# Kernel tuning notes

Hardware: AMD Instinct MI355X
Metric: run time of the kernel (lower is better)

Reference implementation:

```python
import jax, jax.numpy as jnp
import numpy as np

N = 20000       # nodes
E = 320000      # edges (before self-loops)
F_IN = 1024     # num_features
H = 4           # head_num
C = 64          # hidden_size
NC = 4          # n_classes
NEG_SLOPE = 0.2 # PyG GATConv default


def setup_inputs() -> dict:
    key = jax.random.key(0)
    ks = jax.random.split(key, 16)
    def w(k, shape, fan_in):
        return jax.random.normal(k, shape, dtype=jnp.float32) / np.sqrt(fan_in)
    x = jax.random.normal(ks[0], (N, F_IN), dtype=jnp.float32)
    edge_index = jax.random.randint(ks[1], (2, E), 0, N, dtype=jnp.int64)
    return {
        "x": x,
        "edge_index": edge_index,
        # layer 1: F_IN -> H*C, concat
        "w1": w(ks[2], (F_IN, H * C), F_IN),
        "as1": w(ks[3], (H, C), C),
        "ad1": w(ks[4], (H, C), C),
        "b1": jnp.zeros((H * C,), jnp.float32),
        # layer 2: H*C -> H*C, concat
        "w2": w(ks[5], (H * C, H * C), H * C),
        "as2": w(ks[6], (H, C), C),
        "ad2": w(ks[7], (H, C), C),
        "b2": jnp.zeros((H * C,), jnp.float32),
        # out layer: H*C -> C, 1 head, concat=False
        "w3": w(ks[8], (H * C, 1 * C), H * C),
        "as3": w(ks[9], (1, C), C),
        "ad3": w(ks[10], (1, C), C),
        "b3": jnp.zeros((C,), jnp.float32),
        # classifier
        "wc": w(ks[11], (C, NC), C),
        "bc": jnp.zeros((NC,), jnp.float32),
    }


def gat_layer(x, src, dst, W, a_src, a_dst, bias, concat):
    """PyG GATConv (eval mode, self-loops already added to src/dst)."""
    n = x.shape[0]
    Hh, Cc = a_src.shape
    h = (x @ W).reshape(n, Hh, Cc)                       # [N,H,C]
    al_s = jnp.sum(h * a_src[None], axis=-1)             # [N,H]
    al_d = jnp.sum(h * a_dst[None], axis=-1)             # [N,H]
    e = al_s[src] + al_d[dst]                            # [E,H]
    e = jax.nn.leaky_relu(e, NEG_SLOPE)
    # segment softmax over incoming edges of each destination node
    emax = jax.ops.segment_max(e, dst, num_segments=n)   # [N,H]
    ex = jnp.exp(e - emax[dst])
    denom = jax.ops.segment_sum(ex, dst, num_segments=n) # [N,H]
    alpha = ex / (denom[dst] + 1e-16)                    # [E,H]
    msg = h[src] * alpha[..., None]                      # [E,H,C]
    out = jax.ops.segment_sum(msg, dst, num_segments=n)  # [N,H,C]
    if concat:
        out = out.reshape(n, Hh * Cc)
    else:
        out = out.mean(axis=1)
    return out + bias


def reference(x, edge_index, w1, as1, ad1, b1, w2, as2, ad2, b2,
              w3, as3, ad3, b3, wc, bc):
    n = x.shape[0]
    loop = jnp.arange(n, dtype=edge_index.dtype)
    src = jnp.concatenate([edge_index[0], loop])
    dst = jnp.concatenate([edge_index[1], loop])
    out = jax.nn.relu(gat_layer(x, src, dst, w1, as1, ad1, b1, True))
    out = jax.nn.relu(gat_layer(out, src, dst, w2, as2, ad2, b2, True))
    out = gat_layer(out, src, dst, w3, as3, ad3, b3, False)
    return out @ wc + bc                                  # [N, n_classes]
```

## Files before the change

kernel.cpp:

```cpp
#include <hip/hip_runtime.h>

#define N_NODES 20000
#define N_EDGES 320000
#define ET (N_EDGES + N_NODES)
#define F_IN 1024
#define HC 256
#define NC 4

typedef unsigned short ushort_t;
typedef __attribute__((ext_vector_type(8))) short short8;
typedef __attribute__((ext_vector_type(4))) float f32x4;

__device__ inline ushort_t f2bf(float f) {
    unsigned u = __float_as_uint(f);
    unsigned r = (u + 0x7fffu + ((u >> 16) & 1u)) >> 16;
    return (ushort_t)r;
}
__device__ inline float bf2f(ushort_t u) {
    return __uint_as_float(((unsigned)u) << 16);
}

__device__ inline unsigned cvt_pk_bf16(float lo, float hi) {
    unsigned r;
    asm("v_cvt_pk_bf16_f32 %0, %1, %2" : "=v"(r) : "v"(lo), "v"(hi));
    return r;
}

#define GLOAD16(gp, lp) __builtin_amdgcn_global_load_lds( \
    (const __attribute__((address_space(1))) void*)(gp),  \
    (__attribute__((address_space(3))) void*)(lp), 16, 0, 0)

__global__ void count_kernel(const int* __restrict__ ei, int* __restrict__ counts) {
    int e = blockIdx.x * blockDim.x + threadIdx.x;
    if (e >= ET) return;
    int dst = (e < N_EDGES) ? ei[N_EDGES + e] : (e - N_EDGES);
    atomicAdd(&counts[dst], 1);
}

__global__ void scan_kernel(const int* __restrict__ counts, int* __restrict__ row_ptr,
                            int* __restrict__ cursor) {
    __shared__ int sums[1024];
    int t = threadIdx.x;
    const int per = (N_NODES + 1023) / 1024;
    int b = t * per;
    int e = min(b + per, N_NODES);
    int s = 0;
    for (int i = b; i < e; ++i) s += counts[i];
    sums[t] = s;
    __syncthreads();
    for (int off = 1; off < 1024; off <<= 1) {
        int v = (t >= off) ? sums[t - off] : 0;
        __syncthreads();
        sums[t] += v;
        __syncthreads();
    }
    int run = (t == 0) ? 0 : sums[t - 1];
    for (int i = b; i < e; ++i) {
        row_ptr[i] = run;
        cursor[i]  = run;
        run += counts[i];
    }
    if (t == 0) row_ptr[N_NODES] = ET;
}

__global__ void scatter_kernel(const int* __restrict__ ei, int* __restrict__ cursor,
                               int* __restrict__ col) {
    int e = blockIdx.x * blockDim.x + threadIdx.x;
    if (e >= ET) return;
    int src, dst;
    if (e < N_EDGES) { src = ei[e]; dst = ei[N_EDGES + e]; }
    else             { src = dst = e - N_EDGES; }
    int pos = atomicAdd(&cursor[dst], 1);
    col[pos] = src;
}

__global__ void split_T(const float* __restrict__ in, ushort_t* __restrict__ hi,
                        ushort_t* __restrict__ lo, int K, int Nn) {
    int idx = blockIdx.x * blockDim.x + threadIdx.x;
    if (idx >= K * Nn) return;
    int k = idx / Nn, n = idx - k * Nn;
    float v = in[idx];
    ushort_t h = f2bf(v);
    hi[(size_t)n * K + k] = h;
    lo[(size_t)n * K + k] = f2bf(v - bf2f(h));
}

template<int GY>
__launch_bounds__(256)
__global__ void gemm_f32a(const float* __restrict__ X,
                          const ushort_t* __restrict__ BTh, const ushort_t* __restrict__ BTl,
                          float* __restrict__ C, int M, int K, int NT) {
    constexpr int BM = 64, BN = 64, SM = 32, SN = 32, MF = 2, NF = 2;
    __shared__ __align__(16) ushort_t smem[4 * 64 * 32];
    char* Ash = (char*)smem;
    char* Asl = Ash + 64 * 64;
    char* Bsh = Asl + 64 * 64;
    char* Bsl = Bsh + 64 * 64;

    const int t = threadIdx.x, lane = t & 63, w = t >> 6;
    const int wm = w >> 1, wn = w & 1;
    const int nwg = gridDim.x;
    const int id = blockIdx.x;
    const int q = nwg >> 3, r = nwg & 7;
    const int xcd = id & 7, idx = id >> 3;
    const int logical = (xcd < r ? xcd * (q + 1) : r * (q + 1) + (xcd - r) * q) + idx;
    const int bm = (logical / GY) * BM, bn = (logical % GY) * BN;

    const int arow = w * 16 + (lane >> 2);
    const int achk = lane & 3;
    const int grow = min(bm + arow, M - 1);
    const float* xRow = X + (size_t)grow * K + achk * 8;
    const int aoff = arow * 64 + ((achk ^ ((arow >> 1) & 3)) * 16);

    const int gchunk = ((lane & 3) ^ ((lane >> 3) & 3)) * 16;
    const int brow = w * 16 + (lane >> 2);
    size_t gB = (size_t)(bn + brow) * K * 2 + gchunk;
    int lB = w * 1024;

    f32x4 acc[MF][NF];
    #pragma unroll
    for (int i = 0; i < MF; ++i)
        #pragma unroll
        for (int j = 0; j < NF; ++j) acc[i][j] = (f32x4){0.f, 0.f, 0.f, 0.f};

    const char* Bhb = (const char*)BTh;
    const char* Blb = (const char*)BTl;
    const int c16 = (lane >> 4);

    float4 c0 = *(const float4*)(xRow);
    float4 c1 = *(const float4*)(xRow + 4);
    for (int k0 = 0; k0 < K; k0 += 32) {
        float4 n0, n1;
        if (k0 + 32 < K) {
            n0 = *(const float4*)(xRow + k0 + 32);
            n1 = *(const float4*)(xRow + k0 + 36);
        }
        float vv[8] = {c0.x, c0.y, c0.z, c0.w, c1.x, c1.y, c1.z, c1.w};
        unsigned hp[4], lp[4];
        #pragma unroll
        for (int j = 0; j < 4; ++j) {
            unsigned h = cvt_pk_bf16(vv[2 * j], vv[2 * j + 1]);
            float h0 = __uint_as_float(h << 16);
            float h1 = __uint_as_float(h & 0xFFFF0000u);
            hp[j] = h;
            lp[j] = cvt_pk_bf16(vv[2 * j] - h0, vv[2 * j + 1] - h1);
        }
        *(uint4*)(Ash + aoff) = make_uint4(hp[0], hp[1], hp[2], hp[3]);
        *(uint4*)(Asl + aoff) = make_uint4(lp[0], lp[1], lp[2], lp[3]);
        size_t kb = (size_t)k0 * 2;
        GLOAD16(Bhb + gB + kb, Bsh + lB);
        GLOAD16(Blb + gB + kb, Bsl + lB);
        __syncthreads();
        short8 afh[MF], afl[MF], bfh[NF], bfl[NF];
        #pragma unroll
        for (int i = 0; i < MF; ++i) {
            int row = wm * SM + i * 16 + (lane & 15);
            int off = row * 64 + ((c16 ^ ((row >> 1) & 3)) * 16);
            afh[i] = *(const short8*)(Ash + off);
            afl[i] = *(const short8*)(Asl + off);
        }
        #pragma unroll
        for (int j = 0; j < NF; ++j) {
            int row = wn * SN + j * 16 + (lane & 15);
            int off = row * 64 + ((c16 ^ ((row >> 1) & 3)) * 16);
            bfh[j] = *(const short8*)(Bsh + off);
            bfl[j] = *(const short8*)(Bsl + off);
        }
        #pragma unroll
        for (int i = 0; i < MF; ++i)
            #pragma unroll
            for (int j = 0; j < NF; ++j) {
                acc[i][j] = __builtin_amdgcn_mfma_f32_16x16x32_bf16(afh[i], bfh[j], acc[i][j], 0, 0, 0);
                acc[i][j] = __builtin_amdgcn_mfma_f32_16x16x32_bf16(afh[i], bfl[j], acc[i][j], 0, 0, 0);
                acc[i][j] = __builtin_amdgcn_mfma_f32_16x16x32_bf16(afl[i], bfh[j], acc[i][j], 0, 0, 0);
            }
        __syncthreads();
        c0 = n0; c1 = n1;
    }
    #pragma unroll
    for (int i = 0; i < MF; ++i) {
        int rbase = bm + wm * SM + i * 16 + (lane >> 4) * 4;
        #pragma unroll
        for (int j = 0; j < NF; ++j) {
            int col = bn + wn * SN + j * 16 + (lane & 15);
            #pragma unroll
            for (int rr = 0; rr < 4; ++rr)
                if (rbase + rr < M) C[(size_t)(rbase + rr) * NT + col] = acc[i][j][rr];
        }
    }
}

template<int BM, int BN, int GY>
__launch_bounds__(256)
__global__ void gemm_mfma(const ushort_t* __restrict__ Ah, const ushort_t* __restrict__ Al,
                          const ushort_t* __restrict__ BTh, const ushort_t* __restrict__ BTl,
                          float* __restrict__ C, int M, int K, int NT) {
    constexpr int SM = BM / 2;
    constexpr int SN = BN / 2;
    constexpr int MF = SM / 16;
    constexpr int NF = SN / 16;
    constexpr int AQ = BM / 64;
    constexpr int BQ = BN / 64;
    __shared__ __align__(16) ushort_t smem[(2 * BM + 2 * BN) * 32];
    char* Ash = (char*)smem;
    char* Asl = Ash + BM * 64;
    char* Bsh = Asl + BM * 64;
    char* Bsl = Bsh + BN * 64;

    const int t = threadIdx.x, lane = t & 63, w = t >> 6;
    const int wm = w >> 1, wn = w & 1;
    const int nwg = gridDim.x;
    const int id = blockIdx.x;
    const int q = nwg >> 3, r = nwg & 7;
    const int xcd = id & 7, idx = id >> 3;
    const int logical = (xcd < r ? xcd * (q + 1) : r * (q + 1) + (xcd - r) * q) + idx;
    const int bm = (logical / GY) * BM, bn = (logical % GY) * BN;
    const int gchunk = ((lane & 3) ^ ((lane >> 3) & 3)) * 16;

    size_t gA[AQ]; int lA[AQ];
    #pragma unroll
    for (int qq = 0; qq < AQ; ++qq) {
        int inst = w * AQ + qq;
        int row  = inst * 16 + (lane >> 2);
        int grow = min(bm + row, M - 1);
        gA[qq] = (size_t)grow * K * 2 + gchunk;
        lA[qq] = inst * 1024;
    }
    size_t gB[BQ]; int lB[BQ];
    #pragma unroll
    for (int qq = 0; qq < BQ; ++qq) {
        int inst = w * BQ + qq;
        int row  = inst * 16 + (lane >> 2);
        gB[qq] = (size_t)(bn + row) * K * 2 + gchunk;
        lB[qq] = inst * 1024;
    }

    f32x4 acc[MF][NF];
    #pragma unroll
    for (int i = 0; i < MF; ++i)
        #pragma unroll
        for (int j = 0; j < NF; ++j) acc[i][j] = (f32x4){0.f, 0.f, 0.f, 0.f};

    const char* Ahb = (const char*)Ah;
    const char* Alb = (const char*)Al;
    const char* Bhb = (const char*)BTh;
    const char* Blb = (const char*)BTl;
    const int c16 = (lane >> 4);

    for (int k0 = 0; k0 < K; k0 += 32) {
        size_t kb = (size_t)k0 * 2;
        #pragma unroll
        for (int qq = 0; qq < AQ; ++qq) {
            GLOAD16(Ahb + gA[qq] + kb, Ash + lA[qq]);
            GLOAD16(Alb + gA[qq] + kb, Asl + lA[qq]);
        }
        #pragma unroll
        for (int qq = 0; qq < BQ; ++qq) {
            GLOAD16(Bhb + gB[qq] + kb, Bsh + lB[qq]);
            GLOAD16(Blb + gB[qq] + kb, Bsl + lB[qq]);
        }
        __syncthreads();
        short8 afh[MF], afl[MF], bfh[NF], bfl[NF];
        #pragma unroll
        for (int i = 0; i < MF; ++i) {
            int row = wm * SM + i * 16 + (lane & 15);
            int off = row * 64 + ((c16 ^ ((row >> 1) & 3)) * 16);
            afh[i] = *(const short8*)(Ash + off);
            afl[i] = *(const short8*)(Asl + off);
        }
        #pragma unroll
        for (int j = 0; j < NF; ++j) {
            int row = wn * SN + j * 16 + (lane & 15);
            int off = row * 64 + ((c16 ^ ((row >> 1) & 3)) * 16);
            bfh[j] = *(const short8*)(Bsh + off);
            bfl[j] = *(const short8*)(Bsl + off);
        }
        #pragma unroll
        for (int i = 0; i < MF; ++i)
            #pragma unroll
            for (int j = 0; j < NF; ++j) {
                acc[i][j] = __builtin_amdgcn_mfma_f32_16x16x32_bf16(afh[i], bfh[j], acc[i][j], 0, 0, 0);
                acc[i][j] = __builtin_amdgcn_mfma_f32_16x16x32_bf16(afh[i], bfl[j], acc[i][j], 0, 0, 0);
                acc[i][j] = __builtin_amdgcn_mfma_f32_16x16x32_bf16(afl[i], bfh[j], acc[i][j], 0, 0, 0);
            }
        __syncthreads();
    }
    #pragma unroll
    for (int i = 0; i < MF; ++i) {
        int rbase = bm + wm * SM + i * 16 + (lane >> 4) * 4;
        #pragma unroll
        for (int j = 0; j < NF; ++j) {
            int col = bn + wn * SN + j * 16 + (lane & 15);
            #pragma unroll
            for (int rr = 0; rr < 4; ++rr)
                if (rbase + rr < M) C[(size_t)(rbase + rr) * NT + col] = acc[i][j][rr];
        }
    }
}

template<int H>
__global__ void al_kernel(const float* __restrict__ h, const float* __restrict__ as_w,
                          const float* __restrict__ ad_w, float* __restrict__ als,
                          float* __restrict__ ald) {
    int n = blockIdx.x;
    int t = threadIdx.x;
    float hv = h[(size_t)n * (H * 64) + t];
    float s = hv * as_w[t];
    float d = hv * ad_w[t];
    #pragma unroll
    for (int off = 32; off > 0; off >>= 1) {
        s += __shfl_down(s, off, 64);
        d += __shfl_down(d, off, 64);
    }
    if ((t & 63) == 0) {
        int head = t >> 6;
        als[n * H + head] = s;
        ald[n * H + head] = d;
    }
}

template<int H>
__launch_bounds__(256)
__global__ void alpha_kernel(const float* __restrict__ als, const float* __restrict__ ald,
                             const int* __restrict__ row_ptr, const int* __restrict__ col,
                             float* __restrict__ alpha) {
    int lane = threadIdx.x & 63, w = threadIdx.x >> 6;
    int dst = blockIdx.x * 4 + w;
    if (dst >= N_NODES) return;
    int beg = row_ptr[dst], deg = row_ptr[dst + 1] - beg;
    constexpr int ES = 64 / H;
    int i_loc = lane / H, hh = lane % H;
    float ad = ald[dst * H + hh];
    float m = -1e30f, den = 0.f;
    for (int base = 0; base < deg; base += ES) {
        int i = base + i_loc;
        if (i < deg) {
            float e = als[col[beg + i] * H + hh] + ad;
            e = (e > 0.f) ? e : 0.2f * e;
            float nm = fmaxf(m, e);
            den = den * __expf(m - nm) + __expf(e - nm);
            m = nm;
        }
    }
    #pragma unroll
    for (int off = H; off < 64; off <<= 1) {
        float mo = __shfl_xor(m, off, 64);
        float dn = __shfl_xor(den, off, 64);
        float nm = fmaxf(m, mo);
        den = den * __expf(m - nm) + dn * __expf(mo - nm);
        m = nm;
    }
    float rden = 1.f / (den + 1e-16f);
    for (int base = 0; base < deg; base += ES) {
        int i = base + i_loc;
        if (i < deg) {
            float e = als[col[beg + i] * H + hh] + ad;
            e = (e > 0.f) ? e : 0.2f * e;
            alpha[(size_t)hh * ET + beg + i] = __expf(e - m) * rden;
        }
    }
}

template<int CT, int CW, int H, bool RELU, bool SPLIT>
__launch_bounds__(256)
__global__ void agg_v3(const float* __restrict__ h, const float* __restrict__ alpha,
                       const int* __restrict__ row_ptr, const int* __restrict__ col,
                       const float* __restrict__ bias,
                       ushort_t* __restrict__ oh, ushort_t* __restrict__ ol,
                       float* __restrict__ of) {
    constexpr int NS  = CT / CW;
    constexpr int LPT = CW / 4;
    constexpr int TPW = 64 / LPT;
    static_assert(NS == H, "slice==head mapping");
    __shared__ int   s_src[4][64];
    __shared__ float s_alp[4][64];
    const int nwg = gridDim.x;
    const int q = nwg >> 3;
    int id = blockIdx.x;
    int logical = (id & 7) * q + (id >> 3);
    int slice = logical / (N_NODES / 4);
    int g = logical - slice * (N_NODES / 4);
    int lane = threadIdx.x & 63, w = threadIdx.x >> 6;
    int dst = g * 4 + w;
    int beg = row_ptr[dst], deg = row_ptr[dst + 1] - beg;
    int team = lane / LPT;
    int cc = (lane & (LPT - 1)) * 4;

    const int*   colP = col + beg;
    const float* aP   = alpha + (size_t)slice * ET + beg;
    const float* hS   = h + slice * CW + cc;

    float4 acc = make_float4(0.f, 0.f, 0.f, 0.f);
    for (int base = 0; base < deg; base += 64) {
        int cnt = min(64, deg - base);
        if (lane < cnt) {
            s_src[w][lane] = colP[base + lane];
            s_alp[w][lane] = aP[base + lane];
        }
        for (int i = team; i < cnt; i += TPW) {
            int   s = s_src[w][i];
            float a = s_alp[w][i];
            float4 hv = *(const float4*)&hS[s * CT];
            acc.x += a * hv.x; acc.y += a * hv.y;
            acc.z += a * hv.z; acc.w += a * hv.w;
        }
    }
    #pragma unroll
    for (int off = LPT; off < 64; off <<= 1) {
        acc.x += __shfl_xor(acc.x, off, 64);
        acc.y += __shfl_xor(acc.y, off, 64);
        acc.z += __shfl_xor(acc.z, off, 64);
        acc.w += __shfl_xor(acc.w, off, 64);
    }
    if (team == 0) {
        int ch = slice * CW + cc;
        float4 bv = *(const float4*)&bias[ch];
        float v0 = acc.x + bv.x, v1 = acc.y + bv.y, v2 = acc.z + bv.z, v3 = acc.w + bv.w;
        if (RELU) {
            v0 = fmaxf(v0, 0.f); v1 = fmaxf(v1, 0.f);
            v2 = fmaxf(v2, 0.f); v3 = fmaxf(v3, 0.f);
        }
        size_t idx = (size_t)dst * CT + ch;
        if (SPLIT) {
            ushort4 h4, l4;
            h4.x = f2bf(v0); l4.x = f2bf(v0 - bf2f(h4.x));
            h4.y = f2bf(v1); l4.y = f2bf(v1 - bf2f(h4.y));
            h4.z = f2bf(v2); l4.z = f2bf(v2 - bf2f(h4.z));
            h4.w = f2bf(v3); l4.w = f2bf(v3 - bf2f(h4.w));
            *(ushort4*)&oh[idx] = h4;
            *(ushort4*)&ol[idx] = l4;
        } else {
            *(float4*)&of[idx] = make_float4(v0, v1, v2, v3);
        }
    }
}

__global__ void classifier_kernel(const float* __restrict__ x, const float* __restrict__ wc,
                                  const float* __restrict__ bc, float* __restrict__ out) {
    int n = blockIdx.x * blockDim.x + threadIdx.x;
    if (n >= N_NODES) return;
    float acc[NC] = {bc[0], bc[1], bc[2], bc[3]};
    for (int c = 0; c < 64; ++c) {
        float xv = x[(size_t)n * 64 + c];
        #pragma unroll
        for (int k = 0; k < NC; ++k) acc[k] += xv * wc[c * NC + k];
    }
    #pragma unroll
    for (int k = 0; k < NC; ++k) out[(size_t)n * NC + k] = acc[k];
}

extern "C" void kernel_launch(void* const* d_in, const int* in_sizes, int n_in,
                              void* d_out, int out_size, void* d_ws, size_t ws_size,
                              hipStream_t stream) {
    const float* x   = (const float*)d_in[0];
    const int*   ei  = (const int*)d_in[1];
    const float* w1  = (const float*)d_in[2];
    const float* as1 = (const float*)d_in[3];
    const float* ad1 = (const float*)d_in[4];
    const float* b1  = (const float*)d_in[5];
    const float* w2  = (const float*)d_in[6];
    const float* as2 = (const float*)d_in[7];
    const float* ad2 = (const float*)d_in[8];
    const float* b2  = (const float*)d_in[9];
    const float* w3  = (const float*)d_in[10];
    const float* as3 = (const float*)d_in[11];
    const float* ad3 = (const float*)d_in[12];
    const float* b3  = (const float*)d_in[13];
    const float* wc  = (const float*)d_in[14];
    const float* bc  = (const float*)d_in[15];
    float* out = (float*)d_out;

    char* ws = (char*)d_ws;
    size_t off = 0;
    auto alloc = [&](size_t bytes) -> char* {
        char* p = ws + off;
        off = (off + bytes + 255) & ~(size_t)255;
        return p;
    };

    int* counts  = (int*)alloc(N_NODES * 4);
    int* cursor  = (int*)alloc(N_NODES * 4);
    int* row_ptr = (int*)alloc((N_NODES + 1) * 4);
    int* colidx  = (int*)alloc(ET * 4);
    float* als   = (float*)alloc(N_NODES * 4 * 4);
    float* ald   = (float*)alloc(N_NODES * 4 * 4);
    float* alpha = (float*)alloc((size_t)4 * ET * 4);
    float* B0    = (float*)alloc((size_t)N_NODES * HC * 4);

    ushort_t* w1Th = (ushort_t*)alloc((size_t)F_IN * HC * 2);
    ushort_t* w1Tl = (ushort_t*)alloc((size_t)F_IN * HC * 2);
    ushort_t* w2Th = (ushort_t*)alloc((size_t)HC * HC * 2);
    ushort_t* w2Tl = (ushort_t*)alloc((size_t)HC * HC * 2);
    ushort_t* w3Th = (ushort_t*)alloc((size_t)HC * 64 * 2);
    ushort_t* w3Tl = (ushort_t*)alloc((size_t)HC * 64 * 2);
    ushort_t* B1h  = (ushort_t*)alloc((size_t)N_NODES * HC * 2);
    ushort_t* B1l  = (ushort_t*)alloc((size_t)N_NODES * HC * 2);
    float*    B1f  = (float*)alloc((size_t)N_NODES * 64 * 4);

    hipMemsetAsync(counts, 0, N_NODES * sizeof(int), stream);
    int eb = (ET + 255) / 256;
    count_kernel<<<eb, 256, 0, stream>>>(ei, counts);
    scan_kernel<<<1, 1024, 0, stream>>>(counts, row_ptr, cursor);
    scatter_kernel<<<eb, 256, 0, stream>>>(ei, cursor, colidx);

    split_T<<<(F_IN * HC + 255) / 256, 256, 0, stream>>>(w1, w1Th, w1Tl, F_IN, HC);
    split_T<<<(HC * HC + 255) / 256, 256, 0, stream>>>(w2, w2Th, w2Tl, HC, HC);
    split_T<<<(HC * 64 + 255) / 256, 256, 0, stream>>>(w3, w3Th, w3Tl, HC, 64);

    const int nwg64 = ((N_NODES + 63) / 64) * (HC / 64);
    const int nblk_dst = N_NODES / 4;
    gemm_f32a<4><<<nwg64, 256, 0, stream>>>(x, w1Th, w1Tl, B0, N_NODES, F_IN, HC);
    al_kernel<4><<<N_NODES, 256, 0, stream>>>(B0, as1, ad1, als, ald);
    alpha_kernel<4><<<nblk_dst, 256, 0, stream>>>(als, ald, row_ptr, colidx, alpha);
    agg_v3<256, 64, 4, true, true><<<4 * nblk_dst, 256, 0, stream>>>(
        B0, alpha, row_ptr, colidx, b1, B1h, B1l, nullptr);
    gemm_mfma<64, 64, 4><<<nwg64, 256, 0, stream>>>(B1h, B1l, w2Th, w2Tl, B0, N_NODES, HC, HC);
    al_kernel<4><<<N_NODES, 256, 0, stream>>>(B0, as2, ad2, als, ald);
    alpha_kernel<4><<<nblk_dst, 256, 0, stream>>>(als, ald, row_ptr, colidx, alpha);
    agg_v3<256, 64, 4, true, true><<<4 * nblk_dst, 256, 0, stream>>>(
        B0, alpha, row_ptr, colidx, b2, B1h, B1l, nullptr);
    const int nwg3 = (N_NODES + 63) / 64;
    gemm_mfma<64, 64, 1><<<nwg3, 256, 0, stream>>>(B1h, B1l, w3Th, w3Tl, B0, N_NODES, HC, 64);
    al_kernel<1><<<N_NODES, 64, 0, stream>>>(B0, as3, ad3, als, ald);
    alpha_kernel<1><<<nblk_dst, 256, 0, stream>>>(als, ald, row_ptr, colidx, alpha);
    agg_v3<64, 64, 1, false, false><<<nblk_dst, 256, 0, stream>>>(
        B0, alpha, row_ptr, colidx, b3, nullptr, nullptr, B1f);
    classifier_kernel<<<(N_NODES + 255) / 256, 256, 0, stream>>>(B1f, wc, bc, out);
}
```

Measured before the change: 311.3 us.

## Double-buffer LDS tiles in both MFMA GEMM kernels to overlap loads with compute

Both GEMM kernels now use two LDS buffers. The next K-slice is staged into one, through direct global-to-LDS loads and, in the fp32-A kernel, bf16 split conversion, while MFMAs consume the other. This drops one __syncthreads per iteration and hides global load latency behind compute. In exchange it doubles LDS use per block, which may reduce occupancy, and gemm_mfma loses its tile-size template parameters.

```diff
diff --git a/kernel.cpp b/kernel.cpp
--- a/kernel.cpp
+++ b/kernel.cpp
@@ -91,11 +91,8 @@
                           const ushort_t* __restrict__ BTh, const ushort_t* __restrict__ BTl,
                           float* __restrict__ C, int M, int K, int NT) {
     constexpr int BM = 64, BN = 64, SM = 32, SN = 32, MF = 2, NF = 2;
-    __shared__ __align__(16) ushort_t smem[4 * 64 * 32];
-    char* Ash = (char*)smem;
-    char* Asl = Ash + 64 * 64;
-    char* Bsh = Asl + 64 * 64;
-    char* Bsl = Bsh + 64 * 64;
+    constexpr int BUFB = 4 * 64 * 64;
+    __shared__ __align__(16) char smem[2 * BUFB];
 
     const int t = threadIdx.x, lane = t & 63, w = t >> 6;
     const int wm = w >> 1, wn = w & 1;
@@ -114,28 +111,22 @@
 
     const int gchunk = ((lane & 3) ^ ((lane >> 3) & 3)) * 16;
     const int brow = w * 16 + (lane >> 2);
-    size_t gB = (size_t)(bn + brow) * K * 2 + gchunk;
-    int lB = w * 1024;
-
-    f32x4 acc[MF][NF];
-    #pragma unroll
-    for (int i = 0; i < MF; ++i)
-        #pragma unroll
-        for (int j = 0; j < NF; ++j) acc[i][j] = (f32x4){0.f, 0.f, 0.f, 0.f};
+    const size_t gB = (size_t)(bn + brow) * K * 2 + gchunk;
+    const int lB = w * 1024;
 
     const char* Bhb = (const char*)BTh;
     const char* Blb = (const char*)BTl;
     const int c16 = (lane >> 4);
-
-    float4 c0 = *(const float4*)(xRow);
-    float4 c1 = *(const float4*)(xRow + 4);
-    for (int k0 = 0; k0 < K; k0 += 32) {
-        float4 n0, n1;
-        if (k0 + 32 < K) {
-            n0 = *(const float4*)(xRow + k0 + 32);
-            n1 = *(const float4*)(xRow + k0 + 36);
-        }
-        float vv[8] = {c0.x, c0.y, c0.z, c0.w, c1.x, c1.y, c1.z, c1.w};
+    const int NTs = K / 32;
+
+    f32x4 acc[MF][NF];
+    #pragma unroll
+    for (int i = 0; i < MF; ++i)
+        #pragma unroll
+        for (int j = 0; j < NF; ++j) acc[i][j] = (f32x4){0.f, 0.f, 0.f, 0.f};
+
+    auto conv_write = [&](char* base, float4 v0, float4 v1) {
+        float vv[8] = {v0.x, v0.y, v0.z, v0.w, v1.x, v1.y, v1.z, v1.w};
         unsigned hp[4], lp[4];
         #pragma unroll
         for (int j = 0; j < 4; ++j) {
@@ -145,26 +136,50 @@
             hp[j] = h;
             lp[j] = cvt_pk_bf16(vv[2 * j] - h0, vv[2 * j + 1] - h1);
         }
-        *(uint4*)(Ash + aoff) = make_uint4(hp[0], hp[1], hp[2], hp[3]);
-        *(uint4*)(Asl + aoff) = make_uint4(lp[0], lp[1], lp[2], lp[3]);
-        size_t kb = (size_t)k0 * 2;
-        GLOAD16(Bhb + gB + kb, Bsh + lB);
-        GLOAD16(Blb + gB + kb, Bsl + lB);
-        __syncthreads();
+        *(uint4*)(base + aoff)        = make_uint4(hp[0], hp[1], hp[2], hp[3]);
+        *(uint4*)(base + 4096 + aoff) = make_uint4(lp[0], lp[1], lp[2], lp[3]);
+    };
+
+    float4 a0 = *(const float4*)(xRow);
+    float4 a1 = *(const float4*)(xRow + 4);
+    conv_write(smem, a0, a1);
+    GLOAD16(Bhb + gB, smem + 8192 + lB);
+    GLOAD16(Blb + gB, smem + 12288 + lB);
+    float4 b0, b1;
+    if (NTs > 1) {
+        b0 = *(const float4*)(xRow + 32);
+        b1 = *(const float4*)(xRow + 36);
+    }
+    __syncthreads();
+
+    for (int ts = 0; ts < NTs; ++ts) {
+        char* cur = smem + (ts & 1) * BUFB;
+        char* nxt = smem + ((ts & 1) ^ 1) * BUFB;
+        float4 c0, c1;
+        if (ts + 2 < NTs) {
+            c0 = *(const float4*)(xRow + (ts + 2) * 32);
+            c1 = *(const float4*)(xRow + (ts + 2) * 32 + 4);
+        }
+        if (ts + 1 < NTs) {
+            conv_write(nxt, b0, b1);
+            size_t kb = (size_t)(ts + 1) * 64;
+            GLOAD16(Bhb + gB + kb, nxt + 8192 + lB);
+            GLOAD16(Blb + gB + kb, nxt + 12288 + lB);
+        }
         short8 afh[MF], afl[MF], bfh[NF], bfl[NF];
         #pragma unroll
         for (int i = 0; i < MF; ++i) {
             int row = wm * SM + i * 16 + (lane & 15);
             int off = row * 64 + ((c16 ^ ((row >> 1) & 3)) * 16);
-            afh[i] = *(const short8*)(Ash + off);
-            afl[i] = *(const short8*)(Asl + off);
+            afh[i] = *(const short8*)(cur + off);
+            afl[i] = *(const short8*)(cur + 4096 + off);
         }
         #pragma unroll
         for (int j = 0; j < NF; ++j) {
             int row = wn * SN + j * 16 + (lane & 15);
             int off = row * 64 + ((c16 ^ ((row >> 1) & 3)) * 16);
-            bfh[j] = *(const short8*)(Bsh + off);
-            bfl[j] = *(const short8*)(Bsl + off);
+            bfh[j] = *(const short8*)(cur + 8192 + off);
+            bfl[j] = *(const short8*)(cur + 12288 + off);
         }
         #pragma unroll
         for (int i = 0; i < MF; ++i)
@@ -175,7 +190,7 @@
                 acc[i][j] = __builtin_amdgcn_mfma_f32_16x16x32_bf16(afl[i], bfh[j], acc[i][j], 0, 0, 0);
             }
         __syncthreads();
-        c0 = n0; c1 = n1;
+        b0 = c0; b1 = c1;
     }
     #pragma unroll
     for (int i = 0; i < MF; ++i) {
@@ -190,22 +205,14 @@
     }
 }
 
-template<int BM, int BN, int GY>
+template<int GY>
 __launch_bounds__(256)
 __global__ void gemm_mfma(const ushort_t* __restrict__ Ah, const ushort_t* __restrict__ Al,
                           const ushort_t* __restrict__ BTh, const ushort_t* __restrict__ BTl,
                           float* __restrict__ C, int M, int K, int NT) {
-    constexpr int SM = BM / 2;
-    constexpr int SN = BN / 2;
-    constexpr int MF = SM / 16;
-    constexpr int NF = SN / 16;
-    constexpr int AQ = BM / 64;
-    constexpr int BQ = BN / 64;
-    __shared__ __align__(16) ushort_t smem[(2 * BM + 2 * BN) * 32];
-    char* Ash = (char*)smem;
-    char* Asl = Ash + BM * 64;
-    char* Bsh = Asl + BM * 64;
-    char* Bsl = Bsh + BN * 64;
+    constexpr int BM = 64, BN = 64, SM = 32, SN = 32, MF = 2, NF = 2;
+    constexpr int BUFB = 4 * 64 * 64;
+    __shared__ __align__(16) char smem[2 * BUFB];
 
     const int t = threadIdx.x, lane = t & 63, w = t >> 6;
     const int wm = w >> 1, wn = w & 1;
@@ -217,63 +224,54 @@
     const int bm = (logical / GY) * BM, bn = (logical % GY) * BN;
     const int gchunk = ((lane & 3) ^ ((lane >> 3) & 3)) * 16;
 
-    size_t gA[AQ]; int lA[AQ];
-    #pragma unroll
-    for (int qq = 0; qq < AQ; ++qq) {
-        int inst = w * AQ + qq;
-        int row  = inst * 16 + (lane >> 2);
-        int grow = min(bm + row, M - 1);
-        gA[qq] = (size_t)grow * K * 2 + gchunk;
-        lA[qq] = inst * 1024;
-    }
-    size_t gB[BQ]; int lB[BQ];
-    #pragma unroll
-    for (int qq = 0; qq < BQ; ++qq) {
-        int inst = w * BQ + qq;
-        int row  = inst * 16 + (lane >> 2);
-        gB[qq] = (size_t)(bn + row) * K * 2 + gchunk;
-        lB[qq] = inst * 1024;
-    }
-
-    f32x4 acc[MF][NF];
-    #pragma unroll
-    for (int i = 0; i < MF; ++i)
-        #pragma unroll
-        for (int j = 0; j < NF; ++j) acc[i][j] = (f32x4){0.f, 0.f, 0.f, 0.f};
+    const int srow = w * 16 + (lane >> 2);
+    const int grow = min(bm + srow, M - 1);
+    const size_t gA = (size_t)grow * K * 2 + gchunk;
+    const size_t gB = (size_t)(bn + srow) * K * 2 + gchunk;
+    const int lS = w * 1024;
 
     const char* Ahb = (const char*)Ah;
     const char* Alb = (const char*)Al;
     const char* Bhb = (const char*)BTh;
     const char* Blb = (const char*)BTl;
     const int c16 = (lane >> 4);
-
-    for (int k0 = 0; k0 < K; k0 += 32) {
-        size_t kb = (size_t)k0 * 2;
-        #pragma unroll
-        for (int qq = 0; qq < AQ; ++qq) {
-            GLOAD16(Ahb + gA[qq] + kb, Ash + lA[qq]);
-            GLOAD16(Alb + gA[qq] + kb, Asl + lA[qq]);
-        }
-        #pragma unroll
-        for (int qq = 0; qq < BQ; ++qq) {
-            GLOAD16(Bhb + gB[qq] + kb, Bsh + lB[qq]);
-            GLOAD16(Blb + gB[qq] + kb, Bsl + lB[qq]);
-        }
-        __syncthreads();
+    const int NTs = K / 32;
+
+    f32x4 acc[MF][NF];
+    #pragma unroll
+    for (int i = 0; i < MF; ++i)
+        #pragma unroll
+        for (int j = 0; j < NF; ++j) acc[i][j] = (f32x4){0.f, 0.f, 0.f, 0.f};
+
+    auto stage = [&](char* base, int ts) {
+        size_t kb = (size_t)ts * 64;
+        GLOAD16(Ahb + gA + kb, base + lS);
+        GLOAD16(Alb + gA + kb, base + 4096 + lS);
+        GLOAD16(Bhb + gB + kb, base + 8192 + lS);
+        GLOAD16(Blb + gB + kb, base + 12288 + lS);
+    };
+
+    stage(smem, 0);
+    __syncthreads();
+
+    for (int ts = 0; ts < NTs; ++ts) {
+        char* cur = smem + (ts & 1) * BUFB;
+        char* nxt = smem + ((ts & 1) ^ 1) * BUFB;
+        if (ts + 1 < NTs) stage(nxt, ts + 1);
         short8 afh[MF], afl[MF], bfh[NF], bfl[NF];
         #pragma unroll
         for (int i = 0; i < MF; ++i) {
             int row = wm * SM + i * 16 + (lane & 15);
             int off = row * 64 + ((c16 ^ ((row >> 1) & 3)) * 16);
-            afh[i] = *(const short8*)(Ash + off);
-            afl[i] = *(const short8*)(Asl + off);
+            afh[i] = *(const short8*)(cur + off);
+            afl[i] = *(const short8*)(cur + 4096 + off);
         }
         #pragma unroll
         for (int j = 0; j < NF; ++j) {
             int row = wn * SN + j * 16 + (lane & 15);
             int off = row * 64 + ((c16 ^ ((row >> 1) & 3)) * 16);
-            bfh[j] = *(const short8*)(Bsh + off);
-            bfl[j] = *(const short8*)(Bsl + off);
+            bfh[j] = *(const short8*)(cur + 8192 + off);
+            bfl[j] = *(const short8*)(cur + 12288 + off);
         }
         #pragma unroll
         for (int i = 0; i < MF; ++i)
@@ -514,13 +512,13 @@
     alpha_kernel<4><<<nblk_dst, 256, 0, stream>>>(als, ald, row_ptr, colidx, alpha);
     agg_v3<256, 64, 4, true, true><<<4 * nblk_dst, 256, 0, stream>>>(
         B0, alpha, row_ptr, colidx, b1, B1h, B1l, nullptr);
-    gemm_mfma<64, 64, 4><<<nwg64, 256, 0, stream>>>(B1h, B1l, w2Th, w2Tl, B0, N_NODES, HC, HC);
+    gemm_mfma<4><<<nwg64, 256, 0, stream>>>(B1h, B1l, w2Th, w2Tl, B0, N_NODES, HC, HC);
     al_kernel<4><<<N_NODES, 256, 0, stream>>>(B0, as2, ad2, als, ald);
     alpha_kernel<4><<<nblk_dst, 256, 0, stream>>>(als, ald, row_ptr, colidx, alpha);
     agg_v3<256, 64, 4, true, true><<<4 * nblk_dst, 256, 0, stream>>>(
         B0, alpha, row_ptr, colidx, b2, B1h, B1l, nullptr);
     const int nwg3 = (N_NODES + 63) / 64;
-    gemm_mfma<64, 64, 1><<<nwg3, 256, 0, stream>>>(B1h, B1l, w3Th, w3Tl, B0, N_NODES, HC, 64);
+    gemm_mfma<1><<<nwg3, 256, 0, stream>>>(B1h, B1l, w3Th, w3Tl, B0, N_NODES, HC, 64);
     al_kernel<1><<<N_NODES, 64, 0, stream>>>(B0, as3, ad3, als, ald);
     alpha_kernel<1><<<nblk_dst, 256, 0, stream>>>(als, ald, row_ptr, colidx, alpha);
     agg_v3<64, 64, 1, false, false><<<nblk_dst, 256, 0, stream>>>(
```

Result: no change. 315.7 us (+1.4%).

## Fuse attention logit computation into GEMM epilogues and enlarge M tile to 128

Applied to the files above, without the earlier changes.

The separate al_kernel launches are removed. The per-head source and destination attention dot products are now computed in the GEMM epilogue: shuffle reductions across lanes, then a shared-memory combine of the two N-warps. Both GEMM kernels also move from 64x64 to 128x64 tiles, with each warp loading two A row groups. This avoids rereading the projected features and saves three launches, at the cost of more registers per thread and fewer workgroups. The epilogue reuses the tile's shared memory after the main loop's closing barrier.

```diff
diff --git a/kernel.cpp b/kernel.cpp
--- a/kernel.cpp
+++ b/kernel.cpp
@@ -85,17 +85,63 @@
     lo[(size_t)n * K + k] = f2bf(v - bf2f(h));
 }
 
-template<int GY>
+#define AL_EPILOGUE()                                                              \
+    {                                                                              \
+        float asv[NF], adv[NF];                                                    \
+        _Pragma("unroll")                                                          \
+        for (int j = 0; j < NF; ++j) {                                             \
+            int col = bn + wn * SN + j * 16 + (lane & 15);                         \
+            asv[j] = as_w[col];                                                    \
+            adv[j] = ad_w[col];                                                    \
+        }                                                                          \
+        float* s_as = (float*)smem;                                   \
+        float* s_ad = (float*)smem + 2 * BM;                                       \
+        _Pragma("unroll")                                                          \
+        for (int i = 0; i < MF; ++i) {                                             \
+            _Pragma("unroll")                                                      \
+            for (int rr = 0; rr < 4; ++rr) {                                       \
+                float ps = 0.f, pd = 0.f;                                          \
+                _Pragma("unroll")                                                  \
+                for (int j = 0; j < NF; ++j) {                                     \
+                    ps += acc[i][j][rr] * asv[j];                                  \
+                    pd += acc[i][j][rr] * adv[j];                                  \
+                }                                                                  \
+                _Pragma("unroll")                                                  \
+                for (int o = 1; o < 16; o <<= 1) {                                 \
+                    ps += __shfl_xor(ps, o, 64);                                   \
+                    pd += __shfl_xor(pd, o, 64);                                   \
+                }                                                                  \
+                if ((lane & 15) == 0) {                                            \
+                    int rl = wm * SM + i * 16 + (lane >> 4) * 4 + rr;              \
+                    s_as[wn * BM + rl] = ps;                                       \
+                    s_ad[wn * BM + rl] = pd;                                       \
+                }                                                                  \
+            }                                                                      \
+        }                                                                          \
+        __syncthreads();                                                           \
+        if (t < BM) {                                                              \
+            int row = bm + t;                                                      \
+            if (row < M) {                                                         \
+                int hb = bn >> 6;                                                  \
+                als[row * H + hb] = s_as[t] + s_as[BM + t];                        \
+                ald[row * H + hb] = s_ad[t] + s_ad[BM + t];                        \
+            }                                                                      \
+        }                                                                          \
+    }
+
+template<int GY, int H>
 __launch_bounds__(256)
 __global__ void gemm_f32a(const float* __restrict__ X,
                           const ushort_t* __restrict__ BTh, const ushort_t* __restrict__ BTl,
-                          float* __restrict__ C, int M, int K, int NT) {
-    constexpr int BM = 64, BN = 64, SM = 32, SN = 32, MF = 2, NF = 2;
-    __shared__ __align__(16) ushort_t smem[4 * 64 * 32];
-    char* Ash = (char*)smem;
-    char* Asl = Ash + 64 * 64;
-    char* Bsh = Asl + 64 * 64;
-    char* Bsl = Bsh + 64 * 64;
+                          float* __restrict__ C, const float* __restrict__ as_w,
+                          const float* __restrict__ ad_w, float* __restrict__ als,
+                          float* __restrict__ ald, int M, int K, int NT) {
+    constexpr int BM = 128, BN = 64, SM = 64, SN = 32, MF = 4, NF = 2;
+    __shared__ __align__(16) char smem[24576];
+    char* Ash = smem;
+    char* Asl = smem + 8192;
+    char* Bsh = smem + 16384;
+    char* Bsl = smem + 20480;
 
     const int t = threadIdx.x, lane = t & 63, w = t >> 6;
     const int wm = w >> 1, wn = w & 1;
@@ -106,47 +152,62 @@
     const int logical = (xcd < r ? xcd * (q + 1) : r * (q + 1) + (xcd - r) * q) + idx;
     const int bm = (logical / GY) * BM, bn = (logical % GY) * BN;
 
-    const int arow = w * 16 + (lane >> 2);
     const int achk = lane & 3;
-    const int grow = min(bm + arow, M - 1);
-    const float* xRow = X + (size_t)grow * K + achk * 8;
-    const int aoff = arow * 64 + ((achk ^ ((arow >> 1) & 3)) * 16);
-
+    const float* xRow[2]; int aoff[2];
+    #pragma unroll
+    for (int qq = 0; qq < 2; ++qq) {
+        int arow = (w * 2 + qq) * 16 + (lane >> 2);
+        int grow = min(bm + arow, M - 1);
+        xRow[qq] = X + (size_t)grow * K + achk * 8;
+        aoff[qq] = arow * 64 + ((achk ^ ((arow >> 1) & 3)) * 16);
+    }
     const int gchunk = ((lane & 3) ^ ((lane >> 3) & 3)) * 16;
     const int brow = w * 16 + (lane >> 2);
-    size_t gB = (size_t)(bn + brow) * K * 2 + gchunk;
-    int lB = w * 1024;
-
-    f32x4 acc[MF][NF];
-    #pragma unroll
-    for (int i = 0; i < MF; ++i)
-        #pragma unroll
-        for (int j = 0; j < NF; ++j) acc[i][j] = (f32x4){0.f, 0.f, 0.f, 0.f};
+    const size_t gB = (size_t)(bn + brow) * K * 2 + gchunk;
+    const int lB = w * 1024;
 
     const char* Bhb = (const char*)BTh;
     const char* Blb = (const char*)BTl;
     const int c16 = (lane >> 4);
 
-    float4 c0 = *(const float4*)(xRow);
-    float4 c1 = *(const float4*)(xRow + 4);
+    f32x4 acc[MF][NF];
+    #pragma unroll
+    for (int i = 0; i < MF; ++i)
+        #pragma unroll
+        for (int j = 0; j < NF; ++j) acc[i][j] = (f32x4){0.f, 0.f, 0.f, 0.f};
+
+    float4 c0[2], c1[2];
+    #pragma unroll
+    for (int qq = 0; qq < 2; ++qq) {
+        c0[qq] = *(const float4*)(xRow[qq]);
+        c1[qq] = *(const float4*)(xRow[qq] + 4);
+    }
+
     for (int k0 = 0; k0 < K; k0 += 32) {
-        float4 n0, n1;
+        float4 n0[2], n1[2];
         if (k0 + 32 < K) {
-            n0 = *(const float4*)(xRow + k0 + 32);
-            n1 = *(const float4*)(xRow + k0 + 36);
-        }
-        float vv[8] = {c0.x, c0.y, c0.z, c0.w, c1.x, c1.y, c1.z, c1.w};
-        unsigned hp[4], lp[4];
-        #pragma unroll
-        for (int j = 0; j < 4; ++j) {
-            unsigned h = cvt_pk_bf16(vv[2 * j], vv[2 * j + 1]);
-            float h0 = __uint_as_float(h << 16);
-            float h1 = __uint_as_float(h & 0xFFFF0000u);
-            hp[j] = h;
-            lp[j] = cvt_pk_bf16(vv[2 * j] - h0, vv[2 * j + 1] - h1);
-        }
-        *(uint4*)(Ash + aoff) = make_uint4(hp[0], hp[1], hp[2], hp[3]);
-        *(uint4*)(Asl + aoff) = make_uint4(lp[0], lp[1], lp[2], lp[3]);
+            #pragma unroll
+            for (int qq = 0; qq < 2; ++qq) {
+                n0[qq] = *(const float4*)(xRow[qq] + k0 + 32);
+                n1[qq] = *(const float4*)(xRow[qq] + k0 + 36);
+            }
+        }
+        #pragma unroll
+        for (int qq = 0; qq < 2; ++qq) {
+            float vv[8] = {c0[qq].x, c0[qq].y, c0[qq].z, c0[qq].w,
+                           c1[qq].x, c1[qq].y, c1[qq].z, c1[qq].w};
+            unsigned hp[4], lp[4];
+            #pragma unroll
+            for (int j = 0; j < 4; ++j) {
+                unsigned h = cvt_pk_bf16(vv[2 * j], vv[2 * j + 1]);
+                float h0 = __uint_as_float(h << 16);
+                float h1 = __uint_as_float(h & 0xFFFF0000u);
+                hp[j] = h;
+                lp[j] = cvt_pk_bf16(vv[2 * j] - h0, vv[2 * j + 1] - h1);
+            }
+            *(uint4*)(Ash + aoff[qq]) = make_uint4(hp[0], hp[1], hp[2], hp[3]);
+            *(uint4*)(Asl + aoff[qq]) = make_uint4(lp[0], lp[1], lp[2], lp[3]);
+        }
         size_t kb = (size_t)k0 * 2;
         GLOAD16(Bhb + gB + kb, Bsh + lB);
         GLOAD16(Blb + gB + kb, Bsl + lB);
@@ -175,7 +236,8 @@
                 acc[i][j] = __builtin_amdgcn_mfma_f32_16x16x32_bf16(afl[i], bfh[j], acc[i][j], 0, 0, 0);
             }
         __syncthreads();
-        c0 = n0; c1 = n1;
+        #pragma unroll
+        for (int qq = 0; qq < 2; ++qq) { c0[qq] = n0[qq]; c1[qq] = n1[qq]; }
     }
     #pragma unroll
     for (int i = 0; i < MF; ++i) {
@@ -188,24 +250,22 @@
                 if (rbase + rr < M) C[(size_t)(rbase + rr) * NT + col] = acc[i][j][rr];
         }
     }
-}
-
-template<int BM, int BN, int GY>
+    AL_EPILOGUE()
+}
+
+template<int GY, int H>
 __launch_bounds__(256)
 __global__ void gemm_mfma(const ushort_t* __restrict__ Ah, const ushort_t* __restrict__ Al,
                           const ushort_t* __restrict__ BTh, const ushort_t* __restrict__ BTl,
-                          float* __restrict__ C, int M, int K, int NT) {
-    constexpr int SM = BM / 2;
-    constexpr int SN = BN / 2;
-    constexpr int MF = SM / 16;
-    constexpr int NF = SN / 16;
-    constexpr int AQ = BM / 64;
-    constexpr int BQ = BN / 64;
-    __shared__ __align__(16) ushort_t smem[(2 * BM + 2 * BN) * 32];
-    char* Ash = (char*)smem;
-    char* Asl = Ash + BM * 64;
-    char* Bsh = Asl + BM * 64;
-    char* Bsl = Bsh + BN * 64;
+                          float* __restrict__ C, const float* __restrict__ as_w,
+                          const float* __restrict__ ad_w, float* __restrict__ als,
+                          float* __restrict__ ald, int M, int K, int NT) {
+    constexpr int BM = 128, BN = 64, SM = 64, SN = 32, MF = 4, NF = 2;
+    __shared__ __align__(16) char smem[24576];
+    char* Ash = smem;
+    char* Asl = smem + 8192;
+    char* Bsh = smem + 16384;
+    char* Bsl = smem + 20480;
 
     const int t = threadIdx.x, lane = t & 63, w = t >> 6;
     const int wm = w >> 1, wn = w & 1;
@@ -217,29 +277,17 @@
     const int bm = (logical / GY) * BM, bn = (logical % GY) * BN;
     const int gchunk = ((lane & 3) ^ ((lane >> 3) & 3)) * 16;
 
-    size_t gA[AQ]; int lA[AQ];
-    #pragma unroll
-    for (int qq = 0; qq < AQ; ++qq) {
-        int inst = w * AQ + qq;
-        int row  = inst * 16 + (lane >> 2);
-        int grow = min(bm + row, M - 1);
+    size_t gA[2]; int lA[2];
+    #pragma unroll
+    for (int qq = 0; qq < 2; ++qq) {
+        int arow = (w * 2 + qq) * 16 + (lane >> 2);
+        int grow = min(bm + arow, M - 1);
         gA[qq] = (size_t)grow * K * 2 + gchunk;
-        lA[qq] = inst * 1024;
-    }
-    size_t gB[BQ]; int lB[BQ];
-    #pragma unroll
-    for (int qq = 0; qq < BQ; ++qq) {
-        int inst = w * BQ + qq;
-        int row  = inst * 16 + (lane >> 2);
-        gB[qq] = (size_t)(bn + row) * K * 2 + gchunk;
-        lB[qq] = inst * 1024;
-    }
-
-    f32x4 acc[MF][NF];
-    #pragma unroll
-    for (int i = 0; i < MF; ++i)
-        #pragma unroll
-        for (int j = 0; j < NF; ++j) acc[i][j] = (f32x4){0.f, 0.f, 0.f, 0.f};
+        lA[qq] = (w * 2 + qq) * 1024;
+    }
+    const int brow = w * 16 + (lane >> 2);
+    const size_t gB = (size_t)(bn + brow) * K * 2 + gchunk;
+    const int lB = w * 1024;
 
     const char* Ahb = (const char*)Ah;
     const char* Alb = (const char*)Al;
@@ -247,18 +295,21 @@
     const char* Blb = (const char*)BTl;
     const int c16 = (lane >> 4);
 
+    f32x4 acc[MF][NF];
+    #pragma unroll
+    for (int i = 0; i < MF; ++i)
+        #pragma unroll
+        for (int j = 0; j < NF; ++j) acc[i][j] = (f32x4){0.f, 0.f, 0.f, 0.f};
+
     for (int k0 = 0; k0 < K; k0 += 32) {
         size_t kb = (size_t)k0 * 2;
         #pragma unroll
-        for (int qq = 0; qq < AQ; ++qq) {
+        for (int qq = 0; qq < 2; ++qq) {
             GLOAD16(Ahb + gA[qq] + kb, Ash + lA[qq]);
             GLOAD16(Alb + gA[qq] + kb, Asl + lA[qq]);
         }
-        #pragma unroll
-        for (int qq = 0; qq < BQ; ++qq) {
-            GLOAD16(Bhb + gB[qq] + kb, Bsh + lB[qq]);
-            GLOAD16(Blb + gB[qq] + kb, Bsl + lB[qq]);
-        }
+        GLOAD16(Bhb + gB + kb, Bsh + lB);
+        GLOAD16(Blb + gB + kb, Bsl + lB);
         __syncthreads();
         short8 afh[MF], afl[MF], bfh[NF], bfl[NF];
         #pragma unroll
@@ -296,27 +347,7 @@
                 if (rbase + rr < M) C[(size_t)(rbase + rr) * NT + col] = acc[i][j][rr];
         }
     }
-}
-
-template<int H>
-__global__ void al_kernel(const float* __restrict__ h, const float* __restrict__ as_w,
-                          const float* __restrict__ ad_w, float* __restrict__ als,
-                          float* __restrict__ ald) {
-    int n = blockIdx.x;
-    int t = threadIdx.x;
-    float hv = h[(size_t)n * (H * 64) + t];
-    float s = hv * as_w[t];
-    float d = hv * ad_w[t];
-    #pragma unroll
-    for (int off = 32; off > 0; off >>= 1) {
-        s += __shfl_down(s, off, 64);
-        d += __shfl_down(d, off, 64);
-    }
-    if ((t & 63) == 0) {
-        int head = t >> 6;
-        als[n * H + head] = s;
-        ald[n * H + head] = d;
-    }
+    AL_EPILOGUE()
 }
 
 template<int H>
@@ -507,21 +538,21 @@
     split_T<<<(HC * HC + 255) / 256, 256, 0, stream>>>(w2, w2Th, w2Tl, HC, HC);
     split_T<<<(HC * 64 + 255) / 256, 256, 0, stream>>>(w3, w3Th, w3Tl, HC, 64);
 
-    const int nwg64 = ((N_NODES + 63) / 64) * (HC / 64);
+    const int nwg128 = ((N_NODES + 127) / 128) * (HC / 64);
     const int nblk_dst = N_NODES / 4;
-    gemm_f32a<4><<<nwg64, 256, 0, stream>>>(x, w1Th, w1Tl, B0, N_NODES, F_IN, HC);
-    al_kernel<4><<<N_NODES, 256, 0, stream>>>(B0, as1, ad1, als, ald);
+    gemm_f32a<4, 4><<<nwg128, 256, 0, stream>>>(x, w1Th, w1Tl, B0, as1, ad1, als, ald,
+                                                N_NODES, F_IN, HC);
     alpha_kernel<4><<<nblk_dst, 256, 0, stream>>>(als, ald, row_ptr, colidx, alpha);
     agg_v3<256, 64, 4, true, true><<<4 * nblk_dst, 256, 0, stream>>>(
         B0, alpha, row_ptr, colidx, b1, B1h, B1l, nullptr);
-    gemm_mfma<64, 64, 4><<<nwg64, 256, 0, stream>>>(B1h, B1l, w2Th, w2Tl, B0, N_NODES, HC, HC);
-    al_kernel<4><<<N_NODES, 256, 0, stream>>>(B0, as2, ad2, als, ald);
+    gemm_mfma<4, 4><<<nwg128, 256, 0, stream>>>(B1h, B1l, w2Th, w2Tl, B0, as2, ad2, als, ald,
+                                                N_NODES, HC, HC);
     alpha_kernel<4><<<nblk_dst, 256, 0, stream>>>(als, ald, row_ptr, colidx, alpha);
     agg_v3<256, 64, 4, true, true><<<4 * nblk_dst, 256, 0, stream>>>(
         B0, alpha, row_ptr, colidx, b2, B1h, B1l, nullptr);
-    const int nwg3 = (N_NODES + 63) / 64;
-    gemm_mfma<64, 64, 1><<<nwg3, 256, 0, stream>>>(B1h, B1l, w3Th, w3Tl, B0, N_NODES, HC, 64);
-    al_kernel<1><<<N_NODES, 64, 0, stream>>>(B0, as3, ad3, als, ald);
+    const int nwg3 = (N_NODES + 127) / 128;
+    gemm_mfma<1, 1><<<nwg3, 256, 0, stream>>>(B1h, B1l, w3Th, w3Tl, B0, as3, ad3, als, ald,
+                                              N_NODES, HC, 64);
     alpha_kernel<1><<<nblk_dst, 256, 0, stream>>>(als, ald, row_ptr, colidx, alpha);
     agg_v3<64, 64, 1, false, false><<<nblk_dst, 256, 0, stream>>>(
         B0, alpha, row_ptr, colidx, b3, nullptr, nullptr, B1f);
```

New measurement: 298.9 us. 1.04x faster.
